# Kernel tuning notes

Measured on AMD Instinct MI355X. Metric: run time of the kernel, lower is better.

The kernel has to match this reference:

```python
import jax, jax.numpy as jnp
import numpy as np

N_PTS = 20000  # points per cloud


def setup_inputs() -> dict:
    key = jax.random.key(0)
    k1, k2 = jax.random.split(key)
    preds = jax.random.normal(k1, (N_PTS, 3), dtype=jnp.float32)
    gts = jax.random.normal(k2, (1, N_PTS, 3), dtype=jnp.float32)
    return {"preds": preds, "gts": gts}


def reference(preds, gts):
    # x = gts: [B, Nx, 3]; y = preds.unsqueeze(0): [1, Ny, 3] (B must be 1 for bmm)
    y = preds[None]                                   # [1, Ny, 3]
    x = gts                                           # [1, Nx, 3]
    xx = jnp.sum(x * x, axis=-1)                      # [1, Nx]  (diag of x x^T)
    yy = jnp.sum(y * y, axis=-1)                      # [1, Ny]
    zz = jnp.einsum('bnd,bmd->bnm', x, y)             # [1, Nx, Ny]
    P = xx[:, :, None] + yy[:, None, :] - 2.0 * zz    # [1, Nx, Ny] squared dists
    dist1 = jnp.min(P, axis=1)                        # [1, Ny] min over gts points
    dist2 = jnp.min(P, axis=2)                        # [1, Nx] min over pred points
    idx1 = jnp.argmin(P, axis=1)                      # [1, Ny]
    idx2 = jnp.argmin(P, axis=2)                      # [1, Nx]
    return dist1, dist2, idx1, idx2
```

## Files before the change

kernel.cpp:

```cpp
#include <hip/hip_runtime.h>

#define N_PTS  20000
#define NG     128
#define NC     (NG * NG)
#define GMIN   (-6.0f)
#define GINV   (NG / 12.0f)
#define MARGIN 5e-4f
#define SSTRIDE (N_PTS / 64)
#define QB79   79

__device__ __forceinline__ float np_self_dot(float x, float y, float z) {
    return __fadd_rn(__fadd_rn(__fmul_rn(x, x), __fmul_rn(y, y)),
                     __fmul_rn(z, z));
}
__device__ __forceinline__ unsigned ordmap(float f) {
    unsigned b = __float_as_uint(f);
    return (b & 0x80000000u) ? ~b : (b | 0x80000000u);
}
__device__ __forceinline__ float invord(unsigned h) {
    return __uint_as_float((h & 0x80000000u) ? (h ^ 0x80000000u) : ~h);
}
__device__ __forceinline__ int cellC(float v) {
    int c = (int)((v - GMIN) * GINV);
    return c < 0 ? 0 : (c > NG - 1 ? NG - 1 : c);
}
__device__ __forceinline__ unsigned long long wave_min_u64(unsigned long long k) {
    #pragma unroll
    for (int m = 1; m < 64; m <<= 1) {
        unsigned long long o = __shfl_xor(k, m, 64);
        k = (o < k) ? o : k;
    }
    return k;
}

#define EVAL(r)                                                            \
    {   float sr = np_self_dot((r).x, (r).y, (r).z);                       \
        float zz = __fadd_rn(__fadd_rn(__fmul_rn(qx, (r).x),               \
                                       __fmul_rn(qy, (r).y)),              \
                             __fmul_rn(qz, (r).z));                        \
        float P  = __fsub_rn(__fadd_rn(sq, sr), __fadd_rn(zz, zz));        \
        unsigned long long kk =                                            \
            ((unsigned long long)ordmap(P) << 32) | __float_as_uint((r).w);\
        key = (kk < key) ? kk : key; }

__device__ __forceinline__ void stream3(
    const float4* __restrict__ rs, int lane,
    int lo0, int c0, int lo1, int c1, int lo2, int c2,
    float qx, float qy, float qz, float sq, unsigned long long& key)
{
    int s01 = c0 + c1, tot = s01 + c2;
    int t = lane;
    if (t < tot) {
        int p = t < c0 ? lo0 + t : t < s01 ? lo1 + (t - c0) : lo2 + (t - s01);
        float4 rc = rs[p];
        for (t += 64; t < tot; t += 64) {
            int pn = t < c0 ? lo0 + t : t < s01 ? lo1 + (t - c0)
                                                : lo2 + (t - s01);
            float4 rn = rs[pn];
            EVAL(rc)
            rc = rn;
        }
        EVAL(rc)
    }
}

__global__ __launch_bounds__(256) void k_hist(
    const float* __restrict__ preds, const float* __restrict__ gts,
    int* __restrict__ cursor)
{
    int t = blockIdx.x * 256 + threadIdx.x;
    if (t >= 2 * N_PTS) return;
    int cl = t / N_PTS, i = t - cl * N_PTS;
    const float* src = cl ? gts : preds;
    int cell = cellC(src[i*3+0]) * NG + cellC(src[i*3+1]);
    atomicAdd(&cursor[cl * NC + cell], 1);
}

__global__ __launch_bounds__(1024) void k_scan(
    int* __restrict__ cursor, int* __restrict__ bstart)
{
    __shared__ int wsum[16];
    __shared__ int wpre[16];
    int cl = blockIdx.x, t = threadIdx.x;
    int wave = t >> 6, lane = t & 63;

    int base = cl * NC + t * 16;
    const int4* c4 = (const int4*)(cursor + base);
    int4 a = c4[0], b = c4[1], c = c4[2], d = c4[3];
    int v[16] = { a.x, a.y, a.z, a.w, b.x, b.y, b.z, b.w,
                  c.x, c.y, c.z, c.w, d.x, d.y, d.z, d.w };
    int s = 0;
    #pragma unroll
    for (int i = 0; i < 16; ++i) s += v[i];

    int ps = s;
    #pragma unroll
    for (int m = 1; m < 64; m <<= 1) {
        int o = __shfl_up(ps, m, 64);
        if (lane >= m) ps += o;
    }
    if (lane == 63) wsum[wave] = ps;
    __syncthreads();
    if (t < 16) {
        int x = wsum[t];
        int px = x;
        #pragma unroll
        for (int m = 1; m < 16; m <<= 1) {
            int o = __shfl_up(px, m, 16);
            if ((t & 15) >= m) px += o;
        }
        wpre[t] = px - x;
    }
    __syncthreads();

    int run = wpre[wave] + (ps - s);
    #pragma unroll
    for (int i = 0; i < 16; ++i) {
        bstart[cl * (NC + 1) + t * 16 + i] = run;
        cursor[base + i] = run;
        run += v[i];
    }
    if (t == 1023) bstart[cl * (NC + 1) + NC] = run;
}

__global__ __launch_bounds__(256) void k_scatter(
    const float* __restrict__ preds, const float* __restrict__ gts,
    int* __restrict__ cursor, float4* __restrict__ sorted)
{
    int t = blockIdx.x * 256 + threadIdx.x;
    if (t >= 2 * N_PTS) return;
    int cl = t / N_PTS, i = t - cl * N_PTS;
    const float* src = cl ? gts : preds;
    float x = src[i*3+0], y = src[i*3+1], z = src[i*3+2];
    int cell = cellC(x) * NG + cellC(y);
    int pos = atomicAdd(&cursor[cl * NC + cell], 1);
    sorted[(size_t)cl * N_PTS + pos] = make_float4(x, y, z, __int_as_float(i));
}

__global__ __launch_bounds__(64) void k_main(
    const float4* __restrict__ sorted, const int* __restrict__ bstart,
    float* __restrict__ out)
{
    int wid  = blockIdx.x;
    int lane = threadIdx.x;
    int dir  = wid / N_PTS;
    int qpos = wid - dir * N_PTS;
    int rcl  = 1 - dir;

    const float4* rs = sorted + (size_t)rcl * N_PTS;
    const int*    cs = bstart + rcl * (NC + 1);

    float4 samp = rs[lane * SSTRIDE];
    float4 qv   = sorted[(size_t)dir * N_PTS + qpos];
    int    origq = __float_as_int(qv.w);
    float qx = qv.x, qy = qv.y, qz = qv.z;
    float sq = np_self_dot(qx, qy, qz);

    unsigned long long key = ~0ULL;
    int l31 = lane & 31;

    int cx = cellC(qx), cy = cellC(qy);
    int sxL = cx > 0 ? cx - 1 : 0, sxR = cx < NG-1 ? cx + 1 : NG-1;
    int syL = cy > 0 ? cy - 1 : 0, syR = cy < NG-1 ? cy + 1 : NG-1;
    int nrs  = sxR - sxL + 1;
    int xrS  = sxL + (l31 < nrs ? l31 : nrs - 1);
    int colS = (lane < 32) ? syL : (syR + 1);
    int bndS = cs[xrS * NG + colS];
    int lo0 = __shfl(bndS, 0, 64), hi0 = __shfl(bndS, 32, 64);
    int lo1 = __shfl(bndS, 1, 64), hi1 = __shfl(bndS, 33, 64);
    int lo2 = __shfl(bndS, 2, 64), hi2 = __shfl(bndS, 34, 64);
    int c0 = hi0 - lo0;
    int c1 = nrs > 1 ? hi1 - lo1 : 0;
    int c2 = nrs > 2 ? hi2 - lo2 : 0;
    stream3(rs, lane, lo0, c0, lo1, c1, lo2, c2, qx, qy, qz, sq, key);
    EVAL(samp)

    key = wave_min_u64(key);
    float W = sqrtf(invord((unsigned)(key >> 32)) + MARGIN);
    int txL = cellC(qx - W), txR = cellC(qx + W);
    int tyL = cellC(qy - W), tyR = cellC(qy + W);
    if (!(txL >= sxL && txR <= sxR && tyL >= syL && tyR <= syR)) {
        int R = txR - txL + 1;
        for (int g = 0; g < R; g += 32) {
            int rows = R - g; if (rows > 32) rows = 32;
            int xr2  = txL + g + (l31 < rows ? l31 : rows - 1);
            int col2 = (lane < 32) ? tyL : (tyR + 1);
            int b2 = cs[xr2 * NG + col2];
            for (int r0 = 0; r0 < rows; r0 += 3) {
                int i1 = r0 + 1 < rows ? r0 + 1 : rows - 1;
                int i2 = r0 + 2 < rows ? r0 + 2 : rows - 1;
                int L0 = __shfl(b2, r0, 64), H0 = __shfl(b2, 32 + r0, 64);
                int L1 = __shfl(b2, i1, 64), H1 = __shfl(b2, 32 + i1, 64);
                int L2 = __shfl(b2, i2, 64), H2 = __shfl(b2, 32 + i2, 64);
                int d0 = H0 - L0;
                int d1 = (r0 + 1 < rows) ? H1 - L1 : 0;
                int d2 = (r0 + 2 < rows) ? H2 - L2 : 0;
                stream3(rs, lane, L0, d0, L1, d1, L2, d2,
                        qx, qy, qz, sq, key);
            }
        }
        key = wave_min_u64(key);
    }

    if (lane == 0) {
        out[dir * N_PTS + origq]       = invord((unsigned)(key >> 32));
        out[(2 + dir) * N_PTS + origq] = (float)(unsigned)(key & 0xFFFFFFFFu);
    }
}

__device__ __forceinline__ float np_pair(float sq, float sr,
                                         float qx, float qy, float qz,
                                         float rx, float ry, float rz) {
    float zz = __fadd_rn(__fadd_rn(__fmul_rn(qx, rx), __fmul_rn(qy, ry)),
                         __fmul_rn(qz, rz));
    return __fsub_rn(__fadd_rn(sq, sr), __fadd_rn(zz, zz));
}

__global__ __launch_bounds__(256) void chamfer_direct_kernel(
    const float* __restrict__ preds, const float* __restrict__ gts,
    float* __restrict__ out)
{
    __shared__ float4 spts[256];
    int bid = blockIdx.x;
    int dir = bid / QB79;
    int qb  = bid - dir * QB79;
    int q   = qb * 256 + threadIdx.x;

    const float* qpts = (dir == 0) ? preds : gts;
    const float* rpts = (dir == 0) ? gts   : preds;

    int qc = (q < N_PTS) ? q : (N_PTS - 1);
    float qx = qpts[qc*3+0], qy = qpts[qc*3+1], qz = qpts[qc*3+2];
    float sq = np_self_dot(qx, qy, qz);
    float best = 3.4e38f;
    int   bidx = 0;

    for (int t = 0; t < N_PTS; t += 256) {
        int cnt = min(256, N_PTS - t);
        __syncthreads();
        if ((int)threadIdx.x < cnt) {
            int j = t + threadIdx.x;
            float rx = rpts[j*3+0], ry = rpts[j*3+1], rz = rpts[j*3+2];
            spts[threadIdx.x] = make_float4(rx, ry, rz, np_self_dot(rx, ry, rz));
        }
        __syncthreads();
        for (int k = 0; k < cnt; ++k) {
            float4 r = spts[k];
            float d = np_pair(sq, r.w, qx, qy, qz, r.x, r.y, r.z);
            if (d < best) { best = d; bidx = t + k; }
        }
    }
    if (q < N_PTS) {
        out[dir * N_PTS + q]       = best;
        out[(2 + dir) * N_PTS + q] = (float)bidx;
    }
}

extern "C" void kernel_launch(void* const* d_in, const int* in_sizes, int n_in,
                              void* d_out, int out_size, void* d_ws, size_t ws_size,
                              hipStream_t stream) {
    const float* preds = (const float*)d_in[0];
    const float* gts   = (const float*)d_in[1];
    float* out = (float*)d_out;

    char* w = (char*)d_ws;
    size_t sorted_b = (size_t)2 * N_PTS * sizeof(float4);
    size_t bstart_b = (size_t)2 * (NC + 1) * sizeof(int);
    size_t cursor_b = (size_t)2 * NC * sizeof(int);
    size_t need = sorted_b + bstart_b + cursor_b;

    if (ws_size >= need) {
        float4* sorted = (float4*)w;
        int* bstart = (int*)(w + sorted_b);
        int* cursor = (int*)(w + sorted_b + bstart_b);

        hipMemsetAsync(cursor, 0, cursor_b, stream);
        k_hist<<<(2 * N_PTS + 255) / 256, 256, 0, stream>>>(preds, gts, cursor);
        k_scan<<<2, 1024, 0, stream>>>(cursor, bstart);
        k_scatter<<<(2 * N_PTS + 255) / 256, 256, 0, stream>>>(
            preds, gts, cursor, sorted);
        k_main<<<2 * N_PTS, 64, 0, stream>>>(sorted, bstart, out);
    } else {
        chamfer_direct_kernel<<<2 * QB79, 256, 0, stream>>>(preds, gts, out);
    }
}
```

Measured before the change: 122.4 us.

## Fuse memset, histogram, scan and scatter into one cooperative grid-synced kernel

Replaces the memset and the separate histogram, scan and scatter kernels with a single cooperative kernel of 157 blocks. Grid-wide syncs separate zeroing, counting, a two-level prefix scan (per-block totals in a small btot buffer) and the scatter. Each point's coordinates and cell stay in registers between phases instead of being reloaded. This removes three launches and the memset, at the cost of four grid barriers and a dependency on cooperative launch support.

```diff
diff --git a/kernel.cpp b/kernel.cpp
--- a/kernel.cpp
+++ b/kernel.cpp
@@ -1,4 +1,7 @@
 #include <hip/hip_runtime.h>
+#include <hip/hip_cooperative_groups.h>
+
+namespace cg = cooperative_groups;
 
 #define N_PTS  20000
 #define NG     128
@@ -7,6 +10,7 @@
 #define GINV   (NG / 12.0f)
 #define MARGIN 5e-4f
 #define SSTRIDE (N_PTS / 64)
+#define NBLK_STAGE 157
 #define QB79   79
 
 __device__ __forceinline__ float np_self_dot(float x, float y, float z) {
@@ -64,77 +68,83 @@
     }
 }
 
-__global__ __launch_bounds__(256) void k_hist(
+__global__ __launch_bounds__(256) void k_stage(
     const float* __restrict__ preds, const float* __restrict__ gts,
-    int* __restrict__ cursor)
-{
+    int* __restrict__ cursor, int* __restrict__ bstart,
+    float4* __restrict__ sorted, int* __restrict__ btot)
+{
+    cg::grid_group grid = cg::this_grid();
+    __shared__ int wtot[4];
     int t = blockIdx.x * 256 + threadIdx.x;
-    if (t >= 2 * N_PTS) return;
-    int cl = t / N_PTS, i = t - cl * N_PTS;
-    const float* src = cl ? gts : preds;
-    int cell = cellC(src[i*3+0]) * NG + cellC(src[i*3+1]);
-    atomicAdd(&cursor[cl * NC + cell], 1);
-}
-
-__global__ __launch_bounds__(1024) void k_scan(
-    int* __restrict__ cursor, int* __restrict__ bstart)
-{
-    __shared__ int wsum[16];
-    __shared__ int wpre[16];
-    int cl = blockIdx.x, t = threadIdx.x;
-    int wave = t >> 6, lane = t & 63;
-
-    int base = cl * NC + t * 16;
-    const int4* c4 = (const int4*)(cursor + base);
-    int4 a = c4[0], b = c4[1], c = c4[2], d = c4[3];
-    int v[16] = { a.x, a.y, a.z, a.w, b.x, b.y, b.z, b.w,
-                  c.x, c.y, c.z, c.w, d.x, d.y, d.z, d.w };
-    int s = 0;
-    #pragma unroll
-    for (int i = 0; i < 16; ++i) s += v[i];
-
-    int ps = s;
-    #pragma unroll
-    for (int m = 1; m < 64; m <<= 1) {
-        int o = __shfl_up(ps, m, 64);
-        if (lane >= m) ps += o;
-    }
-    if (lane == 63) wsum[wave] = ps;
-    __syncthreads();
-    if (t < 16) {
-        int x = wsum[t];
-        int px = x;
+    int lane = threadIdx.x & 63, wav = (int)threadIdx.x >> 6;
+
+    if (t < 2 * NC)
+        __hip_atomic_store(&cursor[t], 0, __ATOMIC_RELAXED,
+                           __HIP_MEMORY_SCOPE_AGENT);
+    grid.sync();
+
+    int cl = 0, i = 0, cell = 0;
+    float x = 0.f, y = 0.f, z = 0.f;
+    bool valid = t < 2 * N_PTS;
+    if (valid) {
+        cl = t / N_PTS; i = t - cl * N_PTS;
+        const float* src = cl ? gts : preds;
+        x = src[i*3+0]; y = src[i*3+1]; z = src[i*3+2];
+        cell = cellC(x) * NG + cellC(y);
+        atomicAdd(&cursor[cl * NC + cell], 1);
+    }
+    grid.sync();
+
+    bool scanb = t < 2 * NC;
+    int texcl = 0, blkexcl = 0;
+    if (scanb) {
+        int cnt = __hip_atomic_load(&cursor[t], __ATOMIC_RELAXED,
+                                    __HIP_MEMORY_SCOPE_AGENT);
+        int ps = cnt;
         #pragma unroll
-        for (int m = 1; m < 16; m <<= 1) {
-            int o = __shfl_up(px, m, 16);
-            if ((t & 15) >= m) px += o;
-        }
-        wpre[t] = px - x;
-    }
-    __syncthreads();
-
-    int run = wpre[wave] + (ps - s);
-    #pragma unroll
-    for (int i = 0; i < 16; ++i) {
-        bstart[cl * (NC + 1) + t * 16 + i] = run;
-        cursor[base + i] = run;
-        run += v[i];
-    }
-    if (t == 1023) bstart[cl * (NC + 1) + NC] = run;
-}
-
-__global__ __launch_bounds__(256) void k_scatter(
-    const float* __restrict__ preds, const float* __restrict__ gts,
-    int* __restrict__ cursor, float4* __restrict__ sorted)
-{
-    int t = blockIdx.x * 256 + threadIdx.x;
-    if (t >= 2 * N_PTS) return;
-    int cl = t / N_PTS, i = t - cl * N_PTS;
-    const float* src = cl ? gts : preds;
-    float x = src[i*3+0], y = src[i*3+1], z = src[i*3+2];
-    int cell = cellC(x) * NG + cellC(y);
-    int pos = atomicAdd(&cursor[cl * NC + cell], 1);
-    sorted[(size_t)cl * N_PTS + pos] = make_float4(x, y, z, __int_as_float(i));
+        for (int m = 1; m < 64; m <<= 1) {
+            int o = __shfl_up(ps, m, 64);
+            if (lane >= m) ps += o;
+        }
+        if (lane == 63) wtot[wav] = ps;
+        texcl = ps - cnt;
+        __syncthreads();
+        int bsum = 0;
+        #pragma unroll
+        for (int wv = 0; wv < 4; ++wv) {
+            int v = wtot[wv];
+            if (wv < wav) blkexcl += v;
+            bsum += v;
+        }
+        if (threadIdx.x == 0)
+            __hip_atomic_store(&btot[blockIdx.x], bsum, __ATOMIC_RELAXED,
+                               __HIP_MEMORY_SCOPE_AGENT);
+    }
+    grid.sync();
+
+    if (scanb) {
+        int c  = (int)blockIdx.x >> 6;
+        int b0 = (int)blockIdx.x & 63;
+        int v = (lane < b0)
+            ? __hip_atomic_load(&btot[(c << 6) + lane], __ATOMIC_RELAXED,
+                                __HIP_MEMORY_SCOPE_AGENT)
+            : 0;
+        #pragma unroll
+        for (int m = 1; m < 64; m <<= 1) v += __shfl_xor(v, m, 64);
+        int run = v + blkexcl + texcl;
+        int ci  = t & (NC - 1);
+        bstart[c * (NC + 1) + ci] = run;
+        __hip_atomic_store(&cursor[t], run, __ATOMIC_RELAXED,
+                           __HIP_MEMORY_SCOPE_AGENT);
+        if (ci == NC - 1) bstart[c * (NC + 1) + NC] = N_PTS;
+    }
+    grid.sync();
+
+    if (valid) {
+        int pos = atomicAdd(&cursor[cl * NC + cell], 1);
+        sorted[(size_t)cl * N_PTS + pos] = make_float4(x, y, z,
+                                                       __int_as_float(i));
+    }
 }
 
 __global__ __launch_bounds__(64) void k_main(
@@ -267,18 +277,19 @@
     size_t sorted_b = (size_t)2 * N_PTS * sizeof(float4);
     size_t bstart_b = (size_t)2 * (NC + 1) * sizeof(int);
     size_t cursor_b = (size_t)2 * NC * sizeof(int);
-    size_t need = sorted_b + bstart_b + cursor_b;
+    size_t btot_b   = 128 * sizeof(int);
+    size_t need = sorted_b + bstart_b + cursor_b + btot_b;
 
     if (ws_size >= need) {
         float4* sorted = (float4*)w;
         int* bstart = (int*)(w + sorted_b);
         int* cursor = (int*)(w + sorted_b + bstart_b);
-
-        hipMemsetAsync(cursor, 0, cursor_b, stream);
-        k_hist<<<(2 * N_PTS + 255) / 256, 256, 0, stream>>>(preds, gts, cursor);
-        k_scan<<<2, 1024, 0, stream>>>(cursor, bstart);
-        k_scatter<<<(2 * N_PTS + 255) / 256, 256, 0, stream>>>(
-            preds, gts, cursor, sorted);
+        int* btot   = (int*)(w + sorted_b + bstart_b + cursor_b);
+
+        void* args[6] = { (void*)&preds, (void*)&gts, (void*)&cursor,
+                          (void*)&bstart, (void*)&sorted, (void*)&btot };
+        hipLaunchCooperativeKernel((void*)k_stage, dim3(NBLK_STAGE),
+                                   dim3(256), args, 0, stream);
         k_main<<<2 * N_PTS, 64, 0, stream>>>(sorted, bstart, out);
     } else {
         chamfer_direct_kernel<<<2 * QB79, 256, 0, stream>>>(preds, gts, out);
```

After: 186.3 us. 52.2% more time.
